# Kernel optimization log

Measured on AMD Instinct MI355X. Metric: run time of the kernel, lower is better.

Reference implementation:

```python
import jax, jax.numpy as jnp
import numpy as np

BITS = 4
GROUP = 128
IN = 4096
OUT = 14336
B = 64
PACK = 32 // BITS          # 8 values per int32
MAXQ = (1 << BITS) - 1     # 15


def setup_inputs() -> dict:
    key = jax.random.key(0)
    k = jax.random.split(key, 5)
    x = jax.random.normal(k[0], (B, IN), dtype=jnp.float32)
    # non-negative int32 so arithmetic right-shift behaves like logical shift
    qweight = jax.random.randint(k[1], (IN // PACK, OUT), 0, 2**31 - 1, dtype=jnp.int32)
    qzeros = jax.random.randint(k[2], (IN // GROUP, OUT // PACK), 0, 2**31 - 1, dtype=jnp.int32)
    scales = jax.random.uniform(k[3], (IN // GROUP, OUT), dtype=jnp.float32,
                                minval=1e-3, maxval=1e-2)
    bias = jax.random.normal(k[4], (OUT,), dtype=jnp.float32) * 0.01
    g_idx = (jnp.arange(IN) // GROUP).astype(jnp.int32)
    return dict(x=x, qweight=qweight, qzeros=qzeros, scales=scales, bias=bias, g_idx=g_idx)


def _dequant(qweight, qzeros, scales, g_idx):
    shifts = jnp.arange(PACK, dtype=jnp.int32) * BITS  # [PACK]
    # unpack weights: [IN//PACK, PACK, OUT] -> [IN, OUT]
    w = (qweight[:, None, :] >> shifts[None, :, None]) & MAXQ
    w = w.reshape(IN, OUT)
    # unpack zeros: [G, OUT//PACK, PACK] -> [G, OUT]; pack() stored (zeros-1), so add 1 back
    z = (qzeros[:, :, None] >> shifts[None, None, :]) & MAXQ
    z = z.reshape(-1, OUT) + 1
    # per-group dequant with arbitrary g_idx (act-order support)
    return scales[g_idx] * (w - z[g_idx]).astype(scales.dtype)


def reference(x, qweight, qzeros, scales, bias, g_idx):
    W = _dequant(qweight, qzeros, scales, g_idx)  # [IN, OUT]
    return x @ W + bias
```

## Files before the change

### kernel.cpp

```cpp
#include <hip/hip_runtime.h>
#include <hip/hip_bf16.h>

using u32 = unsigned int;
using u16 = unsigned short;

typedef __attribute__((ext_vector_type(8))) _Float16 half8;
typedef __attribute__((ext_vector_type(2))) _Float16 half2v;
typedef __attribute__((ext_vector_type(16))) float f32x16;
typedef __attribute__((ext_vector_type(4))) u32 u32x4;

#define IN_K   4096
#define OUT_N  14336
#define SPLITK 4
#define NSTAGE 8
#define OUT_ELEMS (64 * OUT_N)

__global__ __launch_bounds__(256) void prep_kernel(const float* __restrict__ x,
                                                   u16* __restrict__ xs) {
  const int t = blockIdx.x * 256 + threadIdx.x;
  const int c = t >> 6;
  const int r = t & 63;
  const float* px = x + r * IN_K + c * 8;
  const float4 a = *(const float4*)px;
  const float4 b = *(const float4*)(px + 4);
  const float af[4] = {a.x, a.y, a.z, a.w};
  const float bf[4] = {b.x, b.y, b.z, b.w};
  union { u32x4 v; u32 u[4]; } o;
#pragma unroll
  for (int i = 0; i < 4; ++i) {
    const _Float16 hl = (_Float16)af[i];
    const _Float16 hh = (_Float16)bf[i];
    u16 lo, hi;
    __builtin_memcpy(&lo, &hl, 2);
    __builtin_memcpy(&hi, &hh, 2);
    o.u[i] = (u32)lo | ((u32)hi << 16);
  }
  *(u32x4*)(xs + (size_t)t * 8) = o.v;
}

__global__ __launch_bounds__(256) void bias_init_kernel(const float* __restrict__ bias,
                                                        float* __restrict__ out) {
  const int i = (blockIdx.x * 256 + threadIdx.x) * 4;
  const int col = i % OUT_N;
  *(float4*)(out + i) = *(const float4*)(bias + col);
}

__global__ __launch_bounds__(256) void reduce_kernel(const float* __restrict__ part,
                                                     const float* __restrict__ bias,
                                                     float* __restrict__ out) {
  const int bx = blockIdx.x, ry = blockIdx.y, t = threadIdx.x;
  const int row = ry * 8 + (t >> 5);
  const int c4 = (t & 31) * 4;
  const float* p = part + (((size_t)bx * SPLITK) * 64 + row) * 128 + c4;
  float4 r = *(const float4*)(bias + bx * 128 + c4);
#pragma unroll
  for (int by = 0; by < SPLITK; ++by) {
    const float4 a = *(const float4*)(p + (size_t)by * 64 * 128);
    r.x += a.x; r.y += a.y; r.z += a.z; r.w += a.w;
  }
  *(float4*)(out + (size_t)row * OUT_N + bx * 128 + c4) = r;
}

template <bool ATOMIC>
__global__ __launch_bounds__(256, 2) void qgemm_kernel(
    const u32* __restrict__ qw, const u32* __restrict__ qz,
    const float* __restrict__ scal, const u16* __restrict__ xs,
    float* __restrict__ dst) {
  __shared__ u16 alds[2][8192];
  __shared__ u32 qlds[2][2048];
  const int tid = threadIdx.x;
  const int lane = tid & 63;
  const int wv = tid >> 6;
  const int g = lane >> 5;
  const int nn = lane & 31;
  const int bx = blockIdx.x;
  const int by = blockIdx.y;
  const int colabs = bx * 128 + wv * 32 + nn;
  const int chunk0 = by * 128;
  const int grp0 = by * NSTAGE;
  const int zsh = (colabs & 7) * 4;

  f32x16 acc0, acc1;
#pragma unroll
  for (int i = 0; i < 16; ++i) { acc0[i] = 0.f; acc1[i] = 0.f; }

  float sv[NSTAGE]; u32 zv[NSTAGE];
#pragma unroll
  for (int t = 0; t < NSTAGE; ++t) {
    sv[t] = scal[(size_t)(grp0 + t) * OUT_N + colabs];
    zv[t] = qz[(size_t)(grp0 + t) * (OUT_N / 8) + (colabs >> 3)];
  }

  auto issue = [&](int st) {
    const u16* asrc = xs + (size_t)(chunk0 + st * 16) * 512;
    u16* adst = &alds[st & 1][0];
#pragma unroll
    for (int r = 0; r < 4; ++r) {
      const int p = r * 256 + tid;
      __builtin_amdgcn_global_load_lds(
          (const __attribute__((address_space(1))) void*)(asrc + p * 8),
          (__attribute__((address_space(3))) void*)(adst + p * 8), 16, 0, 0);
    }
    u32* qdst = &qlds[st & 1][0];
#pragma unroll
    for (int r = 0; r < 2; ++r) {
      const int p = r * 256 + tid;
      const int j = p >> 5;
      const int cg = p & 31;
      const u32* src = qw + (size_t)(chunk0 + st * 16 + j) * OUT_N
                          + bx * 128 + cg * 4;
      __builtin_amdgcn_global_load_lds(
          (const __attribute__((address_space(1))) void*)src,
          (__attribute__((address_space(3))) void*)(qdst + p * 4), 16, 0, 0);
    }
  };

  issue(0);

#pragma unroll
  for (int st = 0; st < NSTAGE; ++st) {
    if (st == 0) {
      issue(1);
      asm volatile("s_waitcnt vmcnt(6)" ::: "memory");
    } else if (st < NSTAGE - 1) {
      __builtin_amdgcn_s_barrier();
      issue(st + 1);
      asm volatile("s_waitcnt vmcnt(6)" ::: "memory");
    } else {
      __builtin_amdgcn_s_barrier();
      asm volatile("s_waitcnt vmcnt(0)" ::: "memory");
    }
    __builtin_amdgcn_s_barrier();
    asm volatile("" ::: "memory");

    const u32 zq = (zv[st] >> zsh) & 0xFu;
    const u32 hzu = 0x64016401u + zq * 0x00010001u;
    half2v hz; __builtin_memcpy(&hz, &hzu, 4);
    const _Float16 hs = (_Float16)sv[st];
    const half2v s2 = {hs, hs};

    const u16* abuf = &alds[st & 1][0];
    const u32* qbuf = &qlds[st & 1][0];
#pragma unroll
    for (int s = 0; s < 8; ++s) {
      const int cl = s * 2 + g;
      const half8 a0 = *(const half8*)(abuf + (cl * 64 + nn) * 8);
      const half8 a1 = *(const half8*)(abuf + (cl * 64 + nn + 32) * 8);
      const u32 q = qbuf[cl * 128 + wv * 32 + nn];
      const u32 p0 = (q & 0x000F000Fu) | 0x64006400u;
      const u32 p1 = ((q >> 4) & 0x000F000Fu) | 0x64006400u;
      const u32 p2 = ((q >> 8) & 0x000F000Fu) | 0x64006400u;
      const u32 p3 = ((q >> 12) & 0x000F000Fu) | 0x64006400u;
      half2v t0, t1, t2, t3;
      __builtin_memcpy(&t0, &p0, 4);
      __builtin_memcpy(&t1, &p1, 4);
      __builtin_memcpy(&t2, &p2, 4);
      __builtin_memcpy(&t3, &p3, 4);
      union { half8 v; half2v h[4]; } bb;
      bb.h[0] = (t0 - hz) * s2;
      bb.h[1] = (t1 - hz) * s2;
      bb.h[2] = (t2 - hz) * s2;
      bb.h[3] = (t3 - hz) * s2;
      acc0 = __builtin_amdgcn_mfma_f32_32x32x16_f16(a0, bb.v, acc0, 0, 0, 0);
      acc1 = __builtin_amdgcn_mfma_f32_32x32x16_f16(a1, bb.v, acc1, 0, 0, 0);
    }
  }

#pragma unroll
  for (int r = 0; r < 16; ++r) {
    const int row = (r & 3) + 8 * (r >> 2) + 4 * g;
    if (ATOMIC) {
      unsafeAtomicAdd(&dst[(size_t)row * OUT_N + colabs], acc0[r]);
      unsafeAtomicAdd(&dst[(size_t)(row + 32) * OUT_N + colabs], acc1[r]);
    } else {
      float* p = dst + (((size_t)bx * SPLITK + by) * 64) * 128 + wv * 32 + nn;
      p[(size_t)row * 128] = acc0[r];
      p[(size_t)(row + 32) * 128] = acc1[r];
    }
  }
}

extern "C" void kernel_launch(void* const* d_in, const int* in_sizes, int n_in,
                              void* d_out, int out_size, void* d_ws, size_t ws_size,
                              hipStream_t stream) {
  (void)in_sizes; (void)n_in; (void)out_size;
  const float* x    = (const float*)d_in[0];
  const u32*   qw   = (const u32*)d_in[1];
  const u32*   qz   = (const u32*)d_in[2];
  const float* sc   = (const float*)d_in[3];
  const float* bias = (const float*)d_in[4];
  float* out = (float*)d_out;

  const size_t XS_BYTES   = (size_t)64 * IN_K * 2;
  const size_t PART_BYTES = (size_t)SPLITK * 112 * 8192 * 4;
  u16* xs = (u16*)d_ws;

  prep_kernel<<<128, 256, 0, stream>>>(x, xs);

  if (ws_size >= XS_BYTES + PART_BYTES) {
    float* part = (float*)((char*)d_ws + XS_BYTES);
    qgemm_kernel<false><<<dim3(112, SPLITK), 256, 0, stream>>>(qw, qz, sc, xs, part);
    reduce_kernel<<<dim3(112, 8), 256, 0, stream>>>(part, bias, out);
  } else {
    bias_init_kernel<<<896, 256, 0, stream>>>(bias, out);
    qgemm_kernel<true><<<dim3(112, SPLITK), 256, 0, stream>>>(qw, qz, sc, xs, out);
  }
}
```

Baseline: 28.78 us.

## Widen qgemm tile to 256 columns per block and double split-K

Each block now covers 256 output columns, with each wave computing a 64x64 tile from four MFMA accumulators, so every A fragment loaded from LDS is reused across two B tiles. Split-K goes from 4 to 8 with 4 stages per block, which keeps the grid at 448 blocks. The reduce kernel is remapped to the new 256-wide partial layout. The cost is double the partial-sum traffic in the reduce step, more accumulator registers per thread, and a larger LDS weight buffer, all of which could reduce occupancy.

```diff
diff --git a/kernel.cpp b/kernel.cpp
--- a/kernel.cpp
+++ b/kernel.cpp
@@ -11,8 +11,8 @@
 
 #define IN_K   4096
 #define OUT_N  14336
-#define SPLITK 4
-#define NSTAGE 8
+#define SPLITK 8
+#define NSTAGE 4
 #define OUT_ELEMS (64 * OUT_N)
 
 __global__ __launch_bounds__(256) void prep_kernel(const float* __restrict__ x,
@@ -48,17 +48,36 @@
 __global__ __launch_bounds__(256) void reduce_kernel(const float* __restrict__ part,
                                                      const float* __restrict__ bias,
                                                      float* __restrict__ out) {
-  const int bx = blockIdx.x, ry = blockIdx.y, t = threadIdx.x;
+  const int gx = blockIdx.x, ry = blockIdx.y, t = threadIdx.x;
+  const int bx = gx >> 1, half = gx & 1;
   const int row = ry * 8 + (t >> 5);
-  const int c4 = (t & 31) * 4;
-  const float* p = part + (((size_t)bx * SPLITK) * 64 + row) * 128 + c4;
-  float4 r = *(const float4*)(bias + bx * 128 + c4);
+  const int cin = half * 128 + (t & 31) * 4;
+  const float* p = part + (((size_t)bx * SPLITK) * 64 + row) * 256 + cin;
+  float4 r = *(const float4*)(bias + bx * 256 + cin);
 #pragma unroll
   for (int by = 0; by < SPLITK; ++by) {
-    const float4 a = *(const float4*)(p + (size_t)by * 64 * 128);
+    const float4 a = *(const float4*)(p + (size_t)by * 64 * 256);
     r.x += a.x; r.y += a.y; r.z += a.z; r.w += a.w;
   }
-  *(float4*)(out + (size_t)row * OUT_N + bx * 128 + c4) = r;
+  *(float4*)(out + (size_t)row * OUT_N + bx * 256 + cin) = r;
+}
+
+static __device__ __forceinline__ half8 dequant8(u32 q, half2v hz, half2v s2) {
+  const u32 p0 = (q & 0x000F000Fu) | 0x64006400u;
+  const u32 p1 = ((q >> 4) & 0x000F000Fu) | 0x64006400u;
+  const u32 p2 = ((q >> 8) & 0x000F000Fu) | 0x64006400u;
+  const u32 p3 = ((q >> 12) & 0x000F000Fu) | 0x64006400u;
+  half2v t0, t1, t2, t3;
+  __builtin_memcpy(&t0, &p0, 4);
+  __builtin_memcpy(&t1, &p1, 4);
+  __builtin_memcpy(&t2, &p2, 4);
+  __builtin_memcpy(&t3, &p3, 4);
+  union { half8 v; half2v h[4]; } bb;
+  bb.h[0] = (t0 - hz) * s2;
+  bb.h[1] = (t1 - hz) * s2;
+  bb.h[2] = (t2 - hz) * s2;
+  bb.h[3] = (t3 - hz) * s2;
+  return bb.v;
 }
 
 template <bool ATOMIC>
@@ -67,7 +86,7 @@
     const float* __restrict__ scal, const u16* __restrict__ xs,
     float* __restrict__ dst) {
   __shared__ u16 alds[2][8192];
-  __shared__ u32 qlds[2][2048];
+  __shared__ u32 qlds[2][4096];
   const int tid = threadIdx.x;
   const int lane = tid & 63;
   const int wv = tid >> 6;
@@ -75,21 +94,27 @@
   const int nn = lane & 31;
   const int bx = blockIdx.x;
   const int by = blockIdx.y;
-  const int colabs = bx * 128 + wv * 32 + nn;
-  const int chunk0 = by * 128;
+  const int colw = wv * 64;
+  const int col0 = bx * 256 + colw + nn;
+  const int col1 = col0 + 32;
+  const int chunk0 = by * 64;
   const int grp0 = by * NSTAGE;
-  const int zsh = (colabs & 7) * 4;
-
-  f32x16 acc0, acc1;
-#pragma unroll
-  for (int i = 0; i < 16; ++i) { acc0[i] = 0.f; acc1[i] = 0.f; }
-
-  float sv[NSTAGE]; u32 zv[NSTAGE];
+  const int zsh = (nn & 7) * 4;
+
+  f32x16 acc00, acc01, acc10, acc11;
+#pragma unroll
+  for (int i = 0; i < 16; ++i) { acc00[i] = 0.f; acc01[i] = 0.f;
+                                 acc10[i] = 0.f; acc11[i] = 0.f; }
+
+  float sv0[NSTAGE], sv1[NSTAGE]; u32 zv0[NSTAGE], zv1[NSTAGE];
 #pragma unroll
   for (int t = 0; t < NSTAGE; ++t) {
-    sv[t] = scal[(size_t)(grp0 + t) * OUT_N + colabs];
-    zv[t] = qz[(size_t)(grp0 + t) * (OUT_N / 8) + (colabs >> 3)];
-  }
+    sv0[t] = scal[(size_t)(grp0 + t) * OUT_N + col0];
+    sv1[t] = scal[(size_t)(grp0 + t) * OUT_N + col1];
+    zv0[t] = qz[(size_t)(grp0 + t) * (OUT_N / 8) + (col0 >> 3)];
+    zv1[t] = qz[(size_t)(grp0 + t) * (OUT_N / 8) + (col1 >> 3)];
+  }
+  asm volatile("s_waitcnt vmcnt(0)" ::: "memory");
 
   auto issue = [&](int st) {
     const u16* asrc = xs + (size_t)(chunk0 + st * 16) * 512;
@@ -101,16 +126,15 @@
           (const __attribute__((address_space(1))) void*)(asrc + p * 8),
           (__attribute__((address_space(3))) void*)(adst + p * 8), 16, 0, 0);
     }
+    const u32* qsrc = qw + (size_t)(chunk0 + st * 16) * OUT_N + bx * 256;
     u32* qdst = &qlds[st & 1][0];
 #pragma unroll
-    for (int r = 0; r < 2; ++r) {
+    for (int r = 0; r < 4; ++r) {
       const int p = r * 256 + tid;
-      const int j = p >> 5;
-      const int cg = p & 31;
-      const u32* src = qw + (size_t)(chunk0 + st * 16 + j) * OUT_N
-                          + bx * 128 + cg * 4;
+      const int j = p >> 6;
+      const int cg = p & 63;
       __builtin_amdgcn_global_load_lds(
-          (const __attribute__((address_space(1))) void*)src,
+          (const __attribute__((address_space(1))) void*)(qsrc + (size_t)j * OUT_N + cg * 4),
           (__attribute__((address_space(3))) void*)(qdst + p * 4), 16, 0, 0);
     }
   };
@@ -121,11 +145,11 @@
   for (int st = 0; st < NSTAGE; ++st) {
     if (st == 0) {
       issue(1);
-      asm volatile("s_waitcnt vmcnt(6)" ::: "memory");
+      asm volatile("s_waitcnt vmcnt(8)" ::: "memory");
     } else if (st < NSTAGE - 1) {
       __builtin_amdgcn_s_barrier();
       issue(st + 1);
-      asm volatile("s_waitcnt vmcnt(6)" ::: "memory");
+      asm volatile("s_waitcnt vmcnt(8)" ::: "memory");
     } else {
       __builtin_amdgcn_s_barrier();
       asm volatile("s_waitcnt vmcnt(0)" ::: "memory");
@@ -133,11 +157,17 @@
     __builtin_amdgcn_s_barrier();
     asm volatile("" ::: "memory");
 
-    const u32 zq = (zv[st] >> zsh) & 0xFu;
-    const u32 hzu = 0x64016401u + zq * 0x00010001u;
-    half2v hz; __builtin_memcpy(&hz, &hzu, 4);
-    const _Float16 hs = (_Float16)sv[st];
-    const half2v s2 = {hs, hs};
+    const u32 zq0 = (zv0[st] >> zsh) & 0xFu;
+    const u32 zq1 = (zv1[st] >> zsh) & 0xFu;
+    const u32 hzu0 = 0x64016401u + zq0 * 0x00010001u;
+    const u32 hzu1 = 0x64016401u + zq1 * 0x00010001u;
+    half2v hz0, hz1;
+    __builtin_memcpy(&hz0, &hzu0, 4);
+    __builtin_memcpy(&hz1, &hzu1, 4);
+    const _Float16 hs0 = (_Float16)sv0[st];
+    const _Float16 hs1 = (_Float16)sv1[st];
+    const half2v s20 = {hs0, hs0};
+    const half2v s21 = {hs1, hs1};
 
     const u16* abuf = &alds[st & 1][0];
     const u32* qbuf = &qlds[st & 1][0];
@@ -146,36 +176,35 @@
       const int cl = s * 2 + g;
       const half8 a0 = *(const half8*)(abuf + (cl * 64 + nn) * 8);
       const half8 a1 = *(const half8*)(abuf + (cl * 64 + nn + 32) * 8);
-      const u32 q = qbuf[cl * 128 + wv * 32 + nn];
-      const u32 p0 = (q & 0x000F000Fu) | 0x64006400u;
-      const u32 p1 = ((q >> 4) & 0x000F000Fu) | 0x64006400u;
-      const u32 p2 = ((q >> 8) & 0x000F000Fu) | 0x64006400u;
-      const u32 p3 = ((q >> 12) & 0x000F000Fu) | 0x64006400u;
-      half2v t0, t1, t2, t3;
-      __builtin_memcpy(&t0, &p0, 4);
-      __builtin_memcpy(&t1, &p1, 4);
-      __builtin_memcpy(&t2, &p2, 4);
-      __builtin_memcpy(&t3, &p3, 4);
-      union { half8 v; half2v h[4]; } bb;
-      bb.h[0] = (t0 - hz) * s2;
-      bb.h[1] = (t1 - hz) * s2;
-      bb.h[2] = (t2 - hz) * s2;
-      bb.h[3] = (t3 - hz) * s2;
-      acc0 = __builtin_amdgcn_mfma_f32_32x32x16_f16(a0, bb.v, acc0, 0, 0, 0);
-      acc1 = __builtin_amdgcn_mfma_f32_32x32x16_f16(a1, bb.v, acc1, 0, 0, 0);
-    }
-  }
-
-#pragma unroll
-  for (int r = 0; r < 16; ++r) {
-    const int row = (r & 3) + 8 * (r >> 2) + 4 * g;
-    if (ATOMIC) {
-      unsafeAtomicAdd(&dst[(size_t)row * OUT_N + colabs], acc0[r]);
-      unsafeAtomicAdd(&dst[(size_t)(row + 32) * OUT_N + colabs], acc1[r]);
-    } else {
-      float* p = dst + (((size_t)bx * SPLITK + by) * 64) * 128 + wv * 32 + nn;
-      p[(size_t)row * 128] = acc0[r];
-      p[(size_t)(row + 32) * 128] = acc1[r];
+      const u32 q0 = qbuf[cl * 256 + colw + nn];
+      const u32 q1 = qbuf[cl * 256 + colw + nn + 32];
+      const half8 bb0 = dequant8(q0, hz0, s20);
+      const half8 bb1 = dequant8(q1, hz1, s21);
+      acc00 = __builtin_amdgcn_mfma_f32_32x32x16_f16(a0, bb0, acc00, 0, 0, 0);
+      acc10 = __builtin_amdgcn_mfma_f32_32x32x16_f16(a1, bb0, acc10, 0, 0, 0);
+      acc01 = __builtin_amdgcn_mfma_f32_32x32x16_f16(a0, bb1, acc01, 0, 0, 0);
+      acc11 = __builtin_amdgcn_mfma_f32_32x32x16_f16(a1, bb1, acc11, 0, 0, 0);
+    }
+  }
+
+  if (ATOMIC) {
+#pragma unroll
+    for (int r = 0; r < 16; ++r) {
+      const int row = (r & 3) + 8 * (r >> 2) + 4 * g;
+      unsafeAtomicAdd(&dst[(size_t)row * OUT_N + col0], acc00[r]);
+      unsafeAtomicAdd(&dst[(size_t)row * OUT_N + col1], acc01[r]);
+      unsafeAtomicAdd(&dst[(size_t)(row + 32) * OUT_N + col0], acc10[r]);
+      unsafeAtomicAdd(&dst[(size_t)(row + 32) * OUT_N + col1], acc11[r]);
+    }
+  } else {
+    float* p = dst + (((size_t)bx * SPLITK + by) * 64) * 256 + colw + nn;
+#pragma unroll
+    for (int r = 0; r < 16; ++r) {
+      const int row = (r & 3) + 8 * (r >> 2) + 4 * g;
+      p[(size_t)row * 256]        = acc00[r];
+      p[(size_t)row * 256 + 32]   = acc01[r];
+      p[(size_t)(row + 32) * 256]      = acc10[r];
+      p[(size_t)(row + 32) * 256 + 32] = acc11[r];
     }
   }
 }
@@ -192,17 +221,17 @@
   float* out = (float*)d_out;
 
   const size_t XS_BYTES   = (size_t)64 * IN_K * 2;
-  const size_t PART_BYTES = (size_t)SPLITK * 112 * 8192 * 4;
+  const size_t PART_BYTES = (size_t)56 * SPLITK * 64 * 256 * 4;
   u16* xs = (u16*)d_ws;
 
   prep_kernel<<<128, 256, 0, stream>>>(x, xs);
 
   if (ws_size >= XS_BYTES + PART_BYTES) {
     float* part = (float*)((char*)d_ws + XS_BYTES);
-    qgemm_kernel<false><<<dim3(112, SPLITK), 256, 0, stream>>>(qw, qz, sc, xs, part);
+    qgemm_kernel<false><<<dim3(56, SPLITK), 256, 0, stream>>>(qw, qz, sc, xs, part);
     reduce_kernel<<<dim3(112, 8), 256, 0, stream>>>(part, bias, out);
   } else {
     bias_init_kernel<<<896, 256, 0, stream>>>(bias, out);
-    qgemm_kernel<true><<<dim3(112, SPLITK), 256, 0, stream>>>(qw, qz, sc, xs, out);
-  }
-}
+    qgemm_kernel<true><<<dim3(56, SPLITK), 256, 0, stream>>>(qw, qz, sc, xs, out);
+  }
+}
```

Result: slower. 32.21 us (+11.9%).

## Deepen qgemm LDS pipeline to triple buffering with prefetch distance three

Applied to the files above, without the earlier changes.

Changes the shared-memory staging from double to triple buffering so that three stages of activation and packed-weight tiles are in flight. Each slot is refilled after the compute of the stage that used it, and the vmcnt waits are adjusted to match. The scale and zero preloads are drained before the pipeline starts, and the MFMA loop runs at raised wave priority. The cost is more LDS per block, 72KB instead of 48KB, which may reduce occupancy from the requested two blocks per CU.

```diff
diff --git a/kernel.cpp b/kernel.cpp
--- a/kernel.cpp
+++ b/kernel.cpp
@@ -61,13 +61,31 @@
   *(float4*)(out + (size_t)row * OUT_N + bx * 128 + c4) = r;
 }
 
+static __device__ __forceinline__ half8 dequant8(u32 q, half2v hz, half2v s2) {
+  const u32 p0 = (q & 0x000F000Fu) | 0x64006400u;
+  const u32 p1 = ((q >> 4) & 0x000F000Fu) | 0x64006400u;
+  const u32 p2 = ((q >> 8) & 0x000F000Fu) | 0x64006400u;
+  const u32 p3 = ((q >> 12) & 0x000F000Fu) | 0x64006400u;
+  half2v t0, t1, t2, t3;
+  __builtin_memcpy(&t0, &p0, 4);
+  __builtin_memcpy(&t1, &p1, 4);
+  __builtin_memcpy(&t2, &p2, 4);
+  __builtin_memcpy(&t3, &p3, 4);
+  union { half8 v; half2v h[4]; } bb;
+  bb.h[0] = (t0 - hz) * s2;
+  bb.h[1] = (t1 - hz) * s2;
+  bb.h[2] = (t2 - hz) * s2;
+  bb.h[3] = (t3 - hz) * s2;
+  return bb.v;
+}
+
 template <bool ATOMIC>
 __global__ __launch_bounds__(256, 2) void qgemm_kernel(
     const u32* __restrict__ qw, const u32* __restrict__ qz,
     const float* __restrict__ scal, const u16* __restrict__ xs,
     float* __restrict__ dst) {
-  __shared__ u16 alds[2][8192];
-  __shared__ u32 qlds[2][2048];
+  __shared__ u16 alds[3][8192];
+  __shared__ u32 qlds[3][2048];
   const int tid = threadIdx.x;
   const int lane = tid & 63;
   const int wv = tid >> 6;
@@ -78,7 +96,7 @@
   const int colabs = bx * 128 + wv * 32 + nn;
   const int chunk0 = by * 128;
   const int grp0 = by * NSTAGE;
-  const int zsh = (colabs & 7) * 4;
+  const int zsh = (nn & 7) * 4;
 
   f32x16 acc0, acc1;
 #pragma unroll
@@ -90,10 +108,12 @@
     sv[t] = scal[(size_t)(grp0 + t) * OUT_N + colabs];
     zv[t] = qz[(size_t)(grp0 + t) * (OUT_N / 8) + (colabs >> 3)];
   }
+  asm volatile("s_waitcnt vmcnt(0)" ::: "memory");
 
   auto issue = [&](int st) {
+    const int slot = st % 3;
     const u16* asrc = xs + (size_t)(chunk0 + st * 16) * 512;
-    u16* adst = &alds[st & 1][0];
+    u16* adst = &alds[slot][0];
 #pragma unroll
     for (int r = 0; r < 4; ++r) {
       const int p = r * 256 + tid;
@@ -101,7 +121,7 @@
           (const __attribute__((address_space(1))) void*)(asrc + p * 8),
           (__attribute__((address_space(3))) void*)(adst + p * 8), 16, 0, 0);
     }
-    u32* qdst = &qlds[st & 1][0];
+    u32* qdst = &qlds[slot][0];
 #pragma unroll
     for (int r = 0; r < 2; ++r) {
       const int p = r * 256 + tid;
@@ -115,21 +135,16 @@
     }
   };
 
-  issue(0);
+  issue(0); issue(1); issue(2);
 
 #pragma unroll
   for (int st = 0; st < NSTAGE; ++st) {
-    if (st == 0) {
-      issue(1);
+    if (st <= NSTAGE - 3)
+      asm volatile("s_waitcnt vmcnt(12)" ::: "memory");
+    else if (st == NSTAGE - 2)
       asm volatile("s_waitcnt vmcnt(6)" ::: "memory");
-    } else if (st < NSTAGE - 1) {
-      __builtin_amdgcn_s_barrier();
-      issue(st + 1);
-      asm volatile("s_waitcnt vmcnt(6)" ::: "memory");
-    } else {
-      __builtin_amdgcn_s_barrier();
+    else
       asm volatile("s_waitcnt vmcnt(0)" ::: "memory");
-    }
     __builtin_amdgcn_s_barrier();
     asm volatile("" ::: "memory");
 
@@ -139,30 +154,26 @@
     const _Float16 hs = (_Float16)sv[st];
     const half2v s2 = {hs, hs};
 
-    const u16* abuf = &alds[st & 1][0];
-    const u32* qbuf = &qlds[st & 1][0];
+    const int slot = st % 3;
+    const u16* abuf = &alds[slot][0];
+    const u32* qbuf = &qlds[slot][0];
+    __builtin_amdgcn_s_setprio(1);
 #pragma unroll
     for (int s = 0; s < 8; ++s) {
       const int cl = s * 2 + g;
       const half8 a0 = *(const half8*)(abuf + (cl * 64 + nn) * 8);
       const half8 a1 = *(const half8*)(abuf + (cl * 64 + nn + 32) * 8);
       const u32 q = qbuf[cl * 128 + wv * 32 + nn];
-      const u32 p0 = (q & 0x000F000Fu) | 0x64006400u;
-      const u32 p1 = ((q >> 4) & 0x000F000Fu) | 0x64006400u;
-      const u32 p2 = ((q >> 8) & 0x000F000Fu) | 0x64006400u;
-      const u32 p3 = ((q >> 12) & 0x000F000Fu) | 0x64006400u;
-      half2v t0, t1, t2, t3;
-      __builtin_memcpy(&t0, &p0, 4);
-      __builtin_memcpy(&t1, &p1, 4);
-      __builtin_memcpy(&t2, &p2, 4);
-      __builtin_memcpy(&t3, &p3, 4);
-      union { half8 v; half2v h[4]; } bb;
-      bb.h[0] = (t0 - hz) * s2;
-      bb.h[1] = (t1 - hz) * s2;
-      bb.h[2] = (t2 - hz) * s2;
-      bb.h[3] = (t3 - hz) * s2;
-      acc0 = __builtin_amdgcn_mfma_f32_32x32x16_f16(a0, bb.v, acc0, 0, 0, 0);
-      acc1 = __builtin_amdgcn_mfma_f32_32x32x16_f16(a1, bb.v, acc1, 0, 0, 0);
+      const half8 bb = dequant8(q, hz, s2);
+      acc0 = __builtin_amdgcn_mfma_f32_32x32x16_f16(a0, bb, acc0, 0, 0, 0);
+      acc1 = __builtin_amdgcn_mfma_f32_32x32x16_f16(a1, bb, acc1, 0, 0, 0);
+    }
+    __builtin_amdgcn_s_setprio(0);
+
+    if (st + 3 < NSTAGE) {
+      __builtin_amdgcn_s_barrier();
+      asm volatile("" ::: "memory");
+      issue(st + 3);
     }
   }
 
@@ -192,7 +203,7 @@
   float* out = (float*)d_out;
 
   const size_t XS_BYTES   = (size_t)64 * IN_K * 2;
-  const size_t PART_BYTES = (size_t)SPLITK * 112 * 8192 * 4;
+  const size_t PART_BYTES = (size_t)112 * SPLITK * 64 * 128 * 4;
   u16* xs = (u16*)d_ws;
 
   prep_kernel<<<128, 256, 0, stream>>>(x, xs);
```

Measured after the change: 28.86 us. No clear change (+0.3%).

## Split K across wave groups within a block and reduce in LDS

Applied to the files above, without the earlier changes.

The quantized GEMM now uses 512-thread blocks with a grid of 112x2. Two groups of four waves each handle a separate 1024-wide K slice with 16 smaller pipeline stages, and their partial accumulators are summed through LDS before one write per block. This halves the global partial buffer and the reduce kernel's input, and adds s_setprio around the MFMA loop. The trade-off is fewer blocks (224 instead of 448), which may lower occupancy and latency hiding, plus an extra LDS epilogue with two block-wide syncs.

```diff
diff --git a/kernel.cpp b/kernel.cpp
--- a/kernel.cpp
+++ b/kernel.cpp
@@ -11,9 +11,7 @@
 
 #define IN_K   4096
 #define OUT_N  14336
-#define SPLITK 4
-#define NSTAGE 8
-#define OUT_ELEMS (64 * OUT_N)
+#define NST    16
 
 __global__ __launch_bounds__(256) void prep_kernel(const float* __restrict__ x,
                                                    u16* __restrict__ xs) {
@@ -38,6 +36,24 @@
   *(u32x4*)(xs + (size_t)t * 8) = o.v;
 }
 
+static __device__ __forceinline__ half8 dequant8(u32 q, half2v hz, half2v s2) {
+  const u32 p0 = (q & 0x000F000Fu) | 0x64006400u;
+  const u32 p1 = ((q >> 4) & 0x000F000Fu) | 0x64006400u;
+  const u32 p2 = ((q >> 8) & 0x000F000Fu) | 0x64006400u;
+  const u32 p3 = ((q >> 12) & 0x000F000Fu) | 0x64006400u;
+  half2v t0, t1, t2, t3;
+  __builtin_memcpy(&t0, &p0, 4);
+  __builtin_memcpy(&t1, &p1, 4);
+  __builtin_memcpy(&t2, &p2, 4);
+  __builtin_memcpy(&t3, &p3, 4);
+  union { half8 v; half2v h[4]; } bb;
+  bb.h[0] = (t0 - hz) * s2;
+  bb.h[1] = (t1 - hz) * s2;
+  bb.h[2] = (t2 - hz) * s2;
+  bb.h[3] = (t3 - hz) * s2;
+  return bb.v;
+}
+
 __global__ __launch_bounds__(256) void bias_init_kernel(const float* __restrict__ bias,
                                                         float* __restrict__ out) {
   const int i = (blockIdx.x * 256 + threadIdx.x) * 4;
@@ -51,81 +67,81 @@
   const int bx = blockIdx.x, ry = blockIdx.y, t = threadIdx.x;
   const int row = ry * 8 + (t >> 5);
   const int c4 = (t & 31) * 4;
-  const float* p = part + (((size_t)bx * SPLITK) * 64 + row) * 128 + c4;
-  float4 r = *(const float4*)(bias + bx * 128 + c4);
-#pragma unroll
-  for (int by = 0; by < SPLITK; ++by) {
-    const float4 a = *(const float4*)(p + (size_t)by * 64 * 128);
-    r.x += a.x; r.y += a.y; r.z += a.z; r.w += a.w;
-  }
+  const float4 p0 = *(const float4*)(part + ((size_t)bx * 2 + 0) * 8192 + row * 128 + c4);
+  const float4 p1 = *(const float4*)(part + ((size_t)bx * 2 + 1) * 8192 + row * 128 + c4);
+  const float4 bv = *(const float4*)(bias + bx * 128 + c4);
+  float4 r;
+  r.x = bv.x + p0.x + p1.x;
+  r.y = bv.y + p0.y + p1.y;
+  r.z = bv.z + p0.z + p1.z;
+  r.w = bv.w + p0.w + p1.w;
   *(float4*)(out + (size_t)row * OUT_N + bx * 128 + c4) = r;
 }
 
 template <bool ATOMIC>
-__global__ __launch_bounds__(256, 2) void qgemm_kernel(
+__global__ __launch_bounds__(512, 4) void qgemm_kernel(
     const u32* __restrict__ qw, const u32* __restrict__ qz,
     const float* __restrict__ scal, const u16* __restrict__ xs,
     float* __restrict__ dst) {
-  __shared__ u16 alds[2][8192];
-  __shared__ u32 qlds[2][2048];
+  __shared__ alignas(16) char smem[65536];
   const int tid = threadIdx.x;
   const int lane = tid & 63;
-  const int wv = tid >> 6;
   const int g = lane >> 5;
   const int nn = lane & 31;
+  const int wv = tid >> 6;
+  const int kq2 = wv >> 2;
+  const int cs = wv & 3;
+  const int qt = tid & 255;
   const int bx = blockIdx.x;
   const int by = blockIdx.y;
-  const int colabs = bx * 128 + wv * 32 + nn;
-  const int chunk0 = by * 128;
-  const int grp0 = by * NSTAGE;
-  const int zsh = (colabs & 7) * 4;
+  const int colabs = bx * 128 + cs * 32 + nn;
+  const int kbase = (by * 2 + kq2) * 1024;
+  const int rowb = kbase >> 3;
+  const int grp0 = kbase >> 7;
+  const int zsh = (nn & 7) * 4;
+  char* const region = smem + kq2 * 24576;
 
   f32x16 acc0, acc1;
 #pragma unroll
   for (int i = 0; i < 16; ++i) { acc0[i] = 0.f; acc1[i] = 0.f; }
 
-  float sv[NSTAGE]; u32 zv[NSTAGE];
-#pragma unroll
-  for (int t = 0; t < NSTAGE; ++t) {
+  float sv[8]; u32 zv[8];
+#pragma unroll
+  for (int t = 0; t < 8; ++t) {
     sv[t] = scal[(size_t)(grp0 + t) * OUT_N + colabs];
     zv[t] = qz[(size_t)(grp0 + t) * (OUT_N / 8) + (colabs >> 3)];
   }
+  asm volatile("s_waitcnt vmcnt(0)" ::: "memory");
 
   auto issue = [&](int st) {
-    const u16* asrc = xs + (size_t)(chunk0 + st * 16) * 512;
-    u16* adst = &alds[st & 1][0];
-#pragma unroll
-    for (int r = 0; r < 4; ++r) {
-      const int p = r * 256 + tid;
+    char* ab = region + (st & 1) * 8192;
+    char* qb = region + 16384 + (st & 1) * 4096;
+    const u16* asrc = xs + (size_t)(rowb + st * 8) * 512;
+#pragma unroll
+    for (int r = 0; r < 2; ++r) {
+      const int p = r * 256 + qt;
       __builtin_amdgcn_global_load_lds(
           (const __attribute__((address_space(1))) void*)(asrc + p * 8),
-          (__attribute__((address_space(3))) void*)(adst + p * 8), 16, 0, 0);
-    }
-    u32* qdst = &qlds[st & 1][0];
-#pragma unroll
-    for (int r = 0; r < 2; ++r) {
-      const int p = r * 256 + tid;
-      const int j = p >> 5;
-      const int cg = p & 31;
-      const u32* src = qw + (size_t)(chunk0 + st * 16 + j) * OUT_N
-                          + bx * 128 + cg * 4;
-      __builtin_amdgcn_global_load_lds(
-          (const __attribute__((address_space(1))) void*)src,
-          (__attribute__((address_space(3))) void*)(qdst + p * 4), 16, 0, 0);
-    }
+          (__attribute__((address_space(3))) void*)(ab + p * 16), 16, 0, 0);
+    }
+    const int j = qt >> 5, cg = qt & 31;
+    const u32* qsrc = qw + (size_t)(rowb + st * 8 + j) * OUT_N + bx * 128 + cg * 4;
+    __builtin_amdgcn_global_load_lds(
+        (const __attribute__((address_space(1))) void*)qsrc,
+        (__attribute__((address_space(3))) void*)(qb + qt * 16), 16, 0, 0);
   };
 
   issue(0);
 
 #pragma unroll
-  for (int st = 0; st < NSTAGE; ++st) {
+  for (int st = 0; st < NST; ++st) {
     if (st == 0) {
       issue(1);
-      asm volatile("s_waitcnt vmcnt(6)" ::: "memory");
-    } else if (st < NSTAGE - 1) {
+      asm volatile("s_waitcnt vmcnt(3)" ::: "memory");
+    } else if (st < NST - 1) {
       __builtin_amdgcn_s_barrier();
       issue(st + 1);
-      asm volatile("s_waitcnt vmcnt(6)" ::: "memory");
+      asm volatile("s_waitcnt vmcnt(3)" ::: "memory");
     } else {
       __builtin_amdgcn_s_barrier();
       asm volatile("s_waitcnt vmcnt(0)" ::: "memory");
@@ -133,49 +149,62 @@
     __builtin_amdgcn_s_barrier();
     asm volatile("" ::: "memory");
 
-    const u32 zq = (zv[st] >> zsh) & 0xFu;
+    const int gi = st >> 1;
+    const u32 zq = (zv[gi] >> zsh) & 0xFu;
     const u32 hzu = 0x64016401u + zq * 0x00010001u;
     half2v hz; __builtin_memcpy(&hz, &hzu, 4);
-    const _Float16 hs = (_Float16)sv[st];
+    const _Float16 hs = (_Float16)sv[gi];
     const half2v s2 = {hs, hs};
 
-    const u16* abuf = &alds[st & 1][0];
-    const u32* qbuf = &qlds[st & 1][0];
-#pragma unroll
-    for (int s = 0; s < 8; ++s) {
+    const char* ab = region + (st & 1) * 8192;
+    const char* qb = region + 16384 + (st & 1) * 4096;
+    __builtin_amdgcn_s_setprio(1);
+#pragma unroll
+    for (int s = 0; s < 4; ++s) {
       const int cl = s * 2 + g;
-      const half8 a0 = *(const half8*)(abuf + (cl * 64 + nn) * 8);
-      const half8 a1 = *(const half8*)(abuf + (cl * 64 + nn + 32) * 8);
-      const u32 q = qbuf[cl * 128 + wv * 32 + nn];
-      const u32 p0 = (q & 0x000F000Fu) | 0x64006400u;
-      const u32 p1 = ((q >> 4) & 0x000F000Fu) | 0x64006400u;
-      const u32 p2 = ((q >> 8) & 0x000F000Fu) | 0x64006400u;
-      const u32 p3 = ((q >> 12) & 0x000F000Fu) | 0x64006400u;
-      half2v t0, t1, t2, t3;
-      __builtin_memcpy(&t0, &p0, 4);
-      __builtin_memcpy(&t1, &p1, 4);
-      __builtin_memcpy(&t2, &p2, 4);
-      __builtin_memcpy(&t3, &p3, 4);
-      union { half8 v; half2v h[4]; } bb;
-      bb.h[0] = (t0 - hz) * s2;
-      bb.h[1] = (t1 - hz) * s2;
-      bb.h[2] = (t2 - hz) * s2;
-      bb.h[3] = (t3 - hz) * s2;
-      acc0 = __builtin_amdgcn_mfma_f32_32x32x16_f16(a0, bb.v, acc0, 0, 0, 0);
-      acc1 = __builtin_amdgcn_mfma_f32_32x32x16_f16(a1, bb.v, acc1, 0, 0, 0);
-    }
-  }
-
+      const half8 a0 = *(const half8*)(ab + (cl * 64 + nn) * 16);
+      const half8 a1 = *(const half8*)(ab + (cl * 64 + nn + 32) * 16);
+      const u32 q = *(const u32*)(qb + (cl * 128 + cs * 32 + nn) * 4);
+      const half8 bb = dequant8(q, hz, s2);
+      acc0 = __builtin_amdgcn_mfma_f32_32x32x16_f16(a0, bb, acc0, 0, 0, 0);
+      acc1 = __builtin_amdgcn_mfma_f32_32x32x16_f16(a1, bb, acc1, 0, 0, 0);
+    }
+    __builtin_amdgcn_s_setprio(0);
+  }
+
+  __syncthreads();
+  float* ep = (float*)smem + kq2 * 8192;
 #pragma unroll
   for (int r = 0; r < 16; ++r) {
-    const int row = (r & 3) + 8 * (r >> 2) + 4 * g;
-    if (ATOMIC) {
-      unsafeAtomicAdd(&dst[(size_t)row * OUT_N + colabs], acc0[r]);
-      unsafeAtomicAdd(&dst[(size_t)(row + 32) * OUT_N + colabs], acc1[r]);
-    } else {
-      float* p = dst + (((size_t)bx * SPLITK + by) * 64) * 128 + wv * 32 + nn;
-      p[(size_t)row * 128] = acc0[r];
-      p[(size_t)(row + 32) * 128] = acc1[r];
+    const int row0 = (r & 3) + 8 * (r >> 2) + 4 * g;
+    ep[row0 * 128 + cs * 32 + nn] = acc0[r];
+    ep[(row0 + 32) * 128 + cs * 32 + nn] = acc1[r];
+  }
+  __syncthreads();
+  const float* e0 = (const float*)smem;
+  const float* e1 = e0 + 8192;
+  if (ATOMIC) {
+#pragma unroll
+    for (int i = 0; i < 4; ++i) {
+      const int pos = tid * 16 + i * 4;
+      const int row = pos >> 7, col = pos & 127;
+      const float4 a = *(const float4*)(e0 + pos);
+      const float4 b = *(const float4*)(e1 + pos);
+      float* po = dst + (size_t)row * OUT_N + bx * 128 + col;
+      unsafeAtomicAdd(po + 0, a.x + b.x);
+      unsafeAtomicAdd(po + 1, a.y + b.y);
+      unsafeAtomicAdd(po + 2, a.z + b.z);
+      unsafeAtomicAdd(po + 3, a.w + b.w);
+    }
+  } else {
+    float* pout = dst + ((size_t)bx * 2 + by) * 8192;
+#pragma unroll
+    for (int i = 0; i < 4; ++i) {
+      const int pos = tid * 16 + i * 4;
+      const float4 a = *(const float4*)(e0 + pos);
+      const float4 b = *(const float4*)(e1 + pos);
+      float4 r; r.x = a.x + b.x; r.y = a.y + b.y; r.z = a.z + b.z; r.w = a.w + b.w;
+      *(float4*)(pout + pos) = r;
     }
   }
 }
@@ -192,17 +221,17 @@
   float* out = (float*)d_out;
 
   const size_t XS_BYTES   = (size_t)64 * IN_K * 2;
-  const size_t PART_BYTES = (size_t)SPLITK * 112 * 8192 * 4;
+  const size_t PART_BYTES = (size_t)112 * 2 * 8192 * 4;
   u16* xs = (u16*)d_ws;
 
   prep_kernel<<<128, 256, 0, stream>>>(x, xs);
 
   if (ws_size >= XS_BYTES + PART_BYTES) {
     float* part = (float*)((char*)d_ws + XS_BYTES);
-    qgemm_kernel<false><<<dim3(112, SPLITK), 256, 0, stream>>>(qw, qz, sc, xs, part);
+    qgemm_kernel<false><<<dim3(112, 2), 512, 0, stream>>>(qw, qz, sc, xs, part);
     reduce_kernel<<<dim3(112, 8), 256, 0, stream>>>(part, bias, out);
   } else {
     bias_init_kernel<<<896, 256, 0, stream>>>(bias, out);
-    qgemm_kernel<true><<<dim3(112, SPLITK), 256, 0, stream>>>(qw, qz, sc, xs, out);
-  }
-}
+    qgemm_kernel<true><<<dim3(112, 2), 512, 0, stream>>>(qw, qz, sc, xs, out);
+  }
+}
```

New measurement: 29.23 us. Within noise of the previous version (+1.6%).
